# Kernel tuning notes

Hardware: AMD Instinct MI355X
Metric: run time of the kernel (lower is better)

The kernel has to match this reference:

```python
import jax, jax.numpy as jnp
import numpy as np

EPS = 1e-5

def _bn(x, g, b):
    # BatchNorm3d in training mode over (batch, spatial) dims; x: [B, C, N]
    mean = jnp.mean(x, axis=(0, 2), keepdims=True)
    var = jnp.var(x, axis=(0, 2), keepdims=True)
    return g[None, :, None] * (x - mean) * jax.lax.rsqrt(var + EPS) + b[None, :, None]


def setup_inputs() -> dict:
    key = jax.random.key(0)
    ks = jax.random.split(key, 6)
    B, C, N, K, H = 2, 128, 32768, 9, 512
    x = jax.random.normal(ks[0], (B, C, N, 1), dtype=jnp.float32)
    edge_index = jax.random.randint(ks[1], (2, B, N, K), 0, N, dtype=jnp.int32)
    s = 0.05
    return {
        "x": x,
        "edge_index": edge_index,
        "w_mr": jax.random.normal(ks[2], (C, 2 * C), dtype=jnp.float32) * s,
        "b_mr": jnp.zeros((C,), jnp.float32),
        "g_mr": jnp.ones((C,), jnp.float32),
        "be_mr": jnp.zeros((C,), jnp.float32),
        "w1": jax.random.normal(ks[3], (H, C), dtype=jnp.float32) * s,
        "b1": jnp.zeros((H,), jnp.float32),
        "g1": jnp.ones((H,), jnp.float32),
        "be1": jnp.zeros((H,), jnp.float32),
        "w2": jax.random.normal(ks[4], (C, H), dtype=jnp.float32) * s,
        "b2": jnp.zeros((C,), jnp.float32),
        "g2": jnp.ones((C,), jnp.float32),
        "be2": jnp.zeros((C,), jnp.float32),
    }


def reference(x, edge_index, w_mr, b_mr, g_mr, be_mr, w1, b1, g1, be1, w2, b2, g2, be2):
    # x: [B, C, N, 1], edge_index: [2, B, N, K]
    B, C, N, _ = x.shape
    x2 = x[..., 0]  # [B, C, N]

    # batched_index_select: gather node features along N for each (B, N, K) index
    gather = jax.vmap(lambda xb, ib: xb[:, ib])  # ([C,N],[N,K]) -> [C,N,K]
    x_i = gather(x2, edge_index[1])  # [B, C, N, K] center features
    x_j = gather(x2, edge_index[0])  # [B, C, N, K] neighbor features
    rel = jnp.max(x_j - x_i, axis=-1)  # max-relative reduction -> [B, C, N]

    # torch.cat([x.unsqueeze(2), rel.unsqueeze(2)], 2).reshape(B, 2C, N): interleaved channels
    feat = jnp.stack([x2, rel], axis=2).reshape(B, 2 * C, N)

    # BasicConv([2C, C]): Conv3d 1x1 -> BN -> ReLU
    y = jnp.einsum('oc,bcn->bon', w_mr, feat) + b_mr[None, :, None]
    y = jax.nn.relu(_bn(y, g_mr, be_mr))

    # FFN: conv1x1 C->H, BN, ReLU, conv1x1 H->C, BN, residual
    h = jnp.einsum('hc,bcn->bhn', w1, y) + b1[None, :, None]
    h = jax.nn.relu(_bn(h, g1, be1))
    out = jnp.einsum('ch,bhn->bcn', w2, h) + b2[None, :, None]
    out = _bn(out, g2, be2) + y
    return out  # [B, C, N]
```

## Files before the change

### kernel.cpp

```cpp
#include <hip/hip_runtime.h>
#include <hip/hip_bf16.h>
#include <cstddef>
#include <cstdint>

#define BB 2
#define CC 128
#define NN 32768
#define KNBR 9
#define HH 512
#define PP (BB * NN)
#define TWO_C 256
#define EPSBN 1e-5f

typedef __attribute__((ext_vector_type(4))) float f32x4;
typedef __attribute__((ext_vector_type(8))) short s16x8;

__device__ __forceinline__ float bf2f(unsigned int u) {
    return __uint_as_float(u << 16);
}
__device__ __forceinline__ unsigned short f2bf(float f) {
    unsigned int u = __float_as_uint(f);
    u += 0x7fffu + ((u >> 16) & 1u);
    return (unsigned short)(u >> 16);
}

__device__ __forceinline__ s16x8 bnrelu(s16x8 v, f32x4 sa0, f32x4 sa1,
                                        f32x4 sb0, f32x4 sb1) {
    union { s16x8 s; __hip_bfloat162 h[4]; } u;
    u.s = v;
#pragma unroll
    for (int q = 0; q < 4; q++) {
        const float2 f = __bfloat1622float2(u.h[q]);
        const float slo = (q < 2) ? sa0[2 * q] : sa1[2 * q - 4];
        const float shi = (q < 2) ? sa0[2 * q + 1] : sa1[2 * q - 3];
        const float tlo = (q < 2) ? sb0[2 * q] : sb1[2 * q - 4];
        const float thi = (q < 2) ? sb0[2 * q + 1] : sb1[2 * q - 3];
        u.h[q] = __float22bfloat162_rn(make_float2(
            fmaxf(fmaf(slo, f.x, tlo), 0.f), fmaxf(fmaf(shi, f.y, thi), 0.f)));
    }
    return u.s;
}


__global__ __launch_bounds__(256) void transpose_kernel(
    const float* __restrict__ x, unsigned short* __restrict__ xT) {
    __shared__ float t[32][129];
    const int b = blockIdx.y;
    const int n0 = blockIdx.x * 32;
    const int tid = threadIdx.x;
    {
        const int tn = tid % 32;
        const int cq = tid / 32;
        for (int c = cq; c < CC; c += 8)
            t[tn][c] = x[((size_t)b * CC + c) * NN + n0 + tn];
    }
    __syncthreads();
    {
        const int ct = tid % 128;
        const int nq = tid / 128;
        for (int nl = nq; nl < 32; nl += 2)
            xT[((size_t)b * NN + n0 + nl) * CC + ct] = f2bf(t[nl][ct]);
    }
}

__global__ __launch_bounds__(256) void gather_kernel(
    const unsigned short* __restrict__ xT, const int* __restrict__ ei,
    unsigned short* __restrict__ feat) {
    __shared__ unsigned short lds[16 * 264];
    const int p0 = blockIdx.x * 16;
    const int b = p0 >> 15;
    const int n0 = p0 & (NN - 1);
    const int tid = threadIdx.x;
    const int wv = tid >> 6, lane = tid & 63;
    const unsigned short* xb = xT + (size_t)b * NN * CC;

#pragma unroll
    for (int q = 0; q < 4; q++) {
        const int pl = wv * 4 + q;
        const int n = n0 + pl;
        const int* e0 = ei + ((size_t)b * NN + n) * KNBR;
        const int* e1 = ei + ((size_t)(BB + b) * NN + n) * KNBR;
        const unsigned int xv = *(const unsigned int*)(xb + (size_t)n * CC + lane * 2);
        float m0 = -INFINITY, m1 = -INFINITY;
#pragma unroll
        for (int k = 0; k < KNBR; k++) {
            const int j0 = e0[k], j1 = e1[k];
            const unsigned int va = *(const unsigned int*)(xb + (size_t)j0 * CC + lane * 2);
            const unsigned int vb = *(const unsigned int*)(xb + (size_t)j1 * CC + lane * 2);
            m0 = fmaxf(m0, bf2f(va & 0xffffu) - bf2f(vb & 0xffffu));
            m1 = fmaxf(m1, bf2f(va >> 16) - bf2f(vb >> 16));
        }
        ushort4 o;
        o.x = (unsigned short)(xv & 0xffffu);
        o.y = f2bf(m0);
        o.z = (unsigned short)(xv >> 16);
        o.w = f2bf(m1);
        *(ushort4*)(lds + pl * 264 + lane * 4) = o;
    }
    __syncthreads();
#pragma unroll
    for (int pass = 0; pass < 2; pass++) {
        const int s = pass * 256 + tid;
        const int kt = s >> 6, ln = s & 63;
        const int pl = ln & 15, kq = ln >> 4;
        const s16x8 v = *(const s16x8*)(lds + pl * 264 + kt * 32 + kq * 8);
        *(s16x8*)(feat + ((size_t)((p0 >> 4) * 8 + kt) * 64 + ln) * 8) = v;
    }
}

__global__ __launch_bounds__(256) void wconv_kernel(
    const float* __restrict__ w_mr, const float* __restrict__ w1,
    const float* __restrict__ w2, unsigned short* __restrict__ o_mr,
    unsigned short* __restrict__ o1, unsigned short* __restrict__ o2) {
    const int t = blockIdx.x * 256 + threadIdx.x;
    const float* src; unsigned short* dst; int K; int slot;
    if (t < 8192) { src = w1; dst = o1; K = 128; slot = t; }
    else if (t < 16384) { src = w2; dst = o2; K = 512; slot = t - 8192; }
    else if (t < 20480) { src = w_mr; dst = o_mr; K = 256; slot = t - 16384; }
    else return;
    const int lane = slot & 63;
    const int kt = (slot >> 6) % (K / 32);
    const int ot = (slot >> 6) / (K / 32);
    const int oc = ot * 16 + (lane & 15);
    const int k0 = kt * 32 + (lane >> 4) * 8;
    s16x8 v;
#pragma unroll
    for (int j = 0; j < 8; j++) v[j] = (short)f2bf(src[(size_t)oc * K + k0 + j]);
    *(s16x8*)(dst + (size_t)slot * 8) = v;
}

template <int KTOT, int OCB, int OC, bool ACT>
__global__ __launch_bounds__(256) void sgemm_kernel(
    const unsigned short* __restrict__ A,
    const unsigned short* __restrict__ W,
    const float* __restrict__ bias,
    const float* __restrict__ act,
    unsigned short* __restrict__ Cout,
    float* __restrict__ part) {
    constexpr int KT = KTOT / 32;
    constexpr int NTB = OCB / 16;
    constexpr int NTW = NTB / 2;
    constexpr int NL = NTB / 4;
    constexpr int OCT32 = OC / 32;

    __shared__ __align__(16) unsigned short ALDS[4 * KT * 512];
    __shared__ __align__(16) unsigned short WB[2][NTB * 512];

    const int tid = threadIdx.x;
    const int w = tid >> 6, lane = tid & 63;
    const int mw = w >> 1, nw = w & 1;
    const int lm = lane & 15, lg = lane >> 4;
    const int pt0 = blockIdx.x * 4;
    const int ob = blockIdx.y * OCB;

    {
        const unsigned short* Asrc = A + (size_t)pt0 * KT * 512;
        s16x8 ar[KT];
#pragma unroll
        for (int i = 0; i < KT; i++)
            ar[i] = *(const s16x8*)(Asrc + (size_t)(i * 256 + tid) * 8);
        s16x8 wr0[NL];
#pragma unroll
        for (int i = 0; i < NL; i++) {
            const int s = i * 256 + tid, nt = s >> 6, ln = s & 63;
            wr0[i] = *(const s16x8*)(W + ((size_t)(((ob >> 4) + nt) * KT) * 64 + ln) * 8);
        }
#pragma unroll
        for (int i = 0; i < KT; i++)
            *(s16x8*)(ALDS + (size_t)(i * 256 + tid) * 8) = ar[i];
#pragma unroll
        for (int i = 0; i < NL; i++)
            *(s16x8*)(WB[0] + (size_t)(i * 256 + tid) * 8) = wr0[i];
    }
    __syncthreads();

    f32x4 acc[2][NTW] = {};

    for (int kt = 0; kt < KT; kt++) {
        s16x8 wr[NL];
        if (kt + 1 < KT) {
#pragma unroll
            for (int i = 0; i < NL; i++) {
                const int s = i * 256 + tid, nt = s >> 6, ln = s & 63;
                wr[i] = *(const s16x8*)(
                    W + ((size_t)(((ob >> 4) + nt) * KT + kt + 1) * 64 + ln) * 8);
            }
        }
        s16x8 a0 = *(const s16x8*)(ALDS + (size_t)(((mw * 2 + 0) * KT + kt) * 64 + lane) * 8);
        s16x8 a1 = *(const s16x8*)(ALDS + (size_t)(((mw * 2 + 1) * KT + kt) * 64 + lane) * 8);
        if (ACT) {
            const int ke = kt * 32 + lg * 8;
            const f32x4 xa0 = *(const f32x4*)(act + ke);
            const f32x4 xa1 = *(const f32x4*)(act + ke + 4);
            const f32x4 xb0 = *(const f32x4*)(act + KTOT + ke);
            const f32x4 xb1 = *(const f32x4*)(act + KTOT + ke + 4);
            a0 = bnrelu(a0, xa0, xa1, xb0, xb1);
            a1 = bnrelu(a1, xa0, xa1, xb0, xb1);
        }
        const unsigned short* wb = WB[kt & 1];
#pragma unroll
        for (int n = 0; n < NTW; n++) {
            const s16x8 bF = *(const s16x8*)(wb + (size_t)((nw * NTW + n) * 64 + lane) * 8);
            acc[0][n] = __builtin_amdgcn_mfma_f32_16x16x32_bf16(a0, bF, acc[0][n], 0, 0, 0);
            acc[1][n] = __builtin_amdgcn_mfma_f32_16x16x32_bf16(a1, bF, acc[1][n], 0, 0, 0);
        }
        if (kt + 1 < KT) {
#pragma unroll
            for (int i = 0; i < NL; i++)
                *(s16x8*)(WB[(kt + 1) & 1] + (size_t)(i * 256 + tid) * 8) = wr[i];
        }
        __syncthreads();
    }

    float* bs = (float*)ALDS;
    unsigned short* myct = WB[0] + (size_t)w * (NTW / 2) * 512;
    float sA[NTW], sB[NTW], bo[NTW];
#pragma unroll
    for (int n = 0; n < NTW; n++) {
        sA[n] = 0.f; sB[n] = 0.f;
        bo[n] = bias[ob + nw * (OCB / 2) + n * 16 + lm];
    }
#pragma unroll
    for (int mi = 0; mi < 2; mi++) {
        const int ptile = pt0 + mw * 2 + mi;
#pragma unroll
        for (int n = 0; n < NTW; n++) {
            const int lbase = ((n & 1) * 2 + (lm >> 3)) * 16 + lg * 4;
            const int elem = lm & 7;
#pragma unroll
            for (int j = 0; j < 4; j++) {
                const float h = acc[mi][n][j] + bo[n];
                sA[n] += h;
                sB[n] = fmaf(h, h, sB[n]);
                myct[(size_t)((n >> 1) * 64 + lbase + j) * 8 + elem] = f2bf(h);
            }
        }
#pragma unroll
        for (int og = 0; og < NTW / 2; og++) {
            const s16x8 v = *(const s16x8*)(myct + (size_t)(og * 64 + lane) * 8);
            const int oct = ((ob + nw * (OCB / 2)) >> 5) + og;
            *(s16x8*)(Cout + ((size_t)(ptile * OCT32 + oct) * 64 + lane) * 8) = v;
        }
    }
#pragma unroll
    for (int n = 0; n < NTW; n++) {
        float a = sA[n], q = sB[n];
        a += __shfl_xor(a, 16); a += __shfl_xor(a, 32);
        q += __shfl_xor(q, 16); q += __shfl_xor(q, 32);
        if (lg == 0) {
            const int chl = nw * (OCB / 2) + n * 16 + lm;
            bs[(mw * 2 + 0) * OCB + chl] = a;
            bs[(mw * 2 + 1) * OCB + chl] = q;
        }
    }
    __syncthreads();
    if (tid < OCB) {
        const float s = bs[0 * OCB + tid] + bs[2 * OCB + tid];
        const float q = bs[1 * OCB + tid] + bs[3 * OCB + tid];
        const size_t o = ((size_t)blockIdx.y * gridDim.x + blockIdx.x) * 2 * OCB;
        part[o + tid] = s;
        part[o + OCB + tid] = q;
    }
}

template <int OCB, int GX>
__global__ __launch_bounds__(256) void reduce_kernel(
    const float* __restrict__ part, const float* __restrict__ g,
    const float* __restrict__ be, float* __restrict__ act, int OC, float invP) {
    __shared__ float ls[4], lq[4];
    const int c = blockIdx.x;
    const int by = c / OCB, co = c % OCB;
    const int tid = threadIdx.x;
    float s = 0.f, q = 0.f;
#pragma unroll
    for (int i = 0; i < GX / 256; i++) {
        const int bx = i * 256 + tid;
        const size_t o = (size_t)(by * GX + bx) * 2 * OCB;
        s += part[o + co];
        q += part[o + OCB + co];
    }
#pragma unroll
    for (int off = 32; off >= 1; off >>= 1) {
        s += __shfl_xor(s, off);
        q += __shfl_xor(q, off);
    }
    if ((tid & 63) == 0) { ls[tid >> 6] = s; lq[tid >> 6] = q; }
    __syncthreads();
    if (tid == 0) {
        s = ls[0] + ls[1] + ls[2] + ls[3];
        q = lq[0] + lq[1] + lq[2] + lq[3];
        const float mean = s * invP;
        const float var = q * invP - mean * mean;
        const float a = g[c] * rsqrtf(var + EPSBN);
        act[c] = a;
        act[OC + c] = be[c] - mean * a;
    }
}

__global__ __launch_bounds__(256) void final_kernel(
    const unsigned short* __restrict__ yF, const unsigned short* __restrict__ oF,
    const float* __restrict__ act1, const float* __restrict__ act3,
    float* __restrict__ out) {
    __shared__ float t[32][132];
    const int p0 = blockIdx.x * 32;
    const int b = p0 >> 15;
    const int n0 = p0 & (NN - 1);
    const int tid = threadIdx.x;
#pragma unroll
    for (int s = tid; s < 512; s += 256) {
        const int pt = s >> 8;
        const int kt = (s >> 6) & 3;
        const int lane = s & 63;
        const int nl = pt * 16 + (lane & 15);
        const int c0 = kt * 32 + (lane >> 4) * 8;
        const size_t off = ((size_t)(((p0 >> 4) + pt) * 4 + kt) * 64 + lane) * 8;
        const s16x8 yv = *(const s16x8*)(yF + off);
        const s16x8 ov = *(const s16x8*)(oF + off);
        const f32x4 a1lo = *(const f32x4*)(act1 + c0);
        const f32x4 a1hi = *(const f32x4*)(act1 + c0 + 4);
        const f32x4 b1lo = *(const f32x4*)(act1 + CC + c0);
        const f32x4 b1hi = *(const f32x4*)(act1 + CC + c0 + 4);
        const f32x4 a3lo = *(const f32x4*)(act3 + c0);
        const f32x4 a3hi = *(const f32x4*)(act3 + c0 + 4);
        const f32x4 b3lo = *(const f32x4*)(act3 + CC + c0);
        const f32x4 b3hi = *(const f32x4*)(act3 + CC + c0 + 4);
#pragma unroll
        for (int j = 0; j < 8; j++) {
            const float yf = bf2f((unsigned short)yv[j]);
            const float of = bf2f((unsigned short)ov[j]);
            const float a1 = (j < 4) ? a1lo[j] : a1hi[j - 4];
            const float b1 = (j < 4) ? b1lo[j] : b1hi[j - 4];
            const float a3 = (j < 4) ? a3lo[j] : a3hi[j - 4];
            const float b3 = (j < 4) ? b3lo[j] : b3hi[j - 4];
            t[nl][c0 + j] = fmaf(a3, of, b3) + fmaxf(fmaf(a1, yf, b1), 0.f);
        }
    }
    __syncthreads();
    const int tn = tid & 31;
    const int cq = tid >> 5;
    for (int c = cq; c < CC; c += 8)
        out[((size_t)b * CC + c) * NN + n0 + tn] = t[tn][c];
}

extern "C" void kernel_launch(void* const* d_in, const int* in_sizes, int n_in,
                              void* d_out, int out_size, void* d_ws, size_t ws_size,
                              hipStream_t stream) {
    const float* x     = (const float*)d_in[0];
    const int*   ei    = (const int*)d_in[1];
    const float* w_mr  = (const float*)d_in[2];
    const float* b_mr  = (const float*)d_in[3];
    const float* g_mr  = (const float*)d_in[4];
    const float* be_mr = (const float*)d_in[5];
    const float* w1    = (const float*)d_in[6];
    const float* b1    = (const float*)d_in[7];
    const float* g1    = (const float*)d_in[8];
    const float* be1   = (const float*)d_in[9];
    const float* w2    = (const float*)d_in[10];
    const float* b2    = (const float*)d_in[11];
    const float* g2    = (const float*)d_in[12];
    const float* be2   = (const float*)d_in[13];
    float* out = (float*)d_out;

    char* ws = (char*)d_ws;
    unsigned short* xT    = (unsigned short*)(ws + 0);
    unsigned short* featF = (unsigned short*)(ws + 16777216);
    unsigned short* yF    = (unsigned short*)(ws + 50331648);
    unsigned short* hF    = (unsigned short*)(ws + 67108864);
    unsigned short* oF    = (unsigned short*)(ws + 134217728);
    unsigned short* wmrF  = (unsigned short*)(ws + 150994944);
    unsigned short* w1F   = (unsigned short*)(ws + 151060480);
    unsigned short* w2F   = (unsigned short*)(ws + 151191552);
    float* act1  = (float*)(ws + 151322624);
    float* act2  = (float*)(ws + 151323648);
    float* act3  = (float*)(ws + 151327744);
    float* part1 = (float*)(ws + 67108864);
    float* part2 = (float*)(ws + 134217728);
    float* part3 = (float*)(ws + 16777216);

    const float invP = 1.0f / (float)PP;

    transpose_kernel<<<dim3(NN / 32, BB), 256, 0, stream>>>(x, xT);
    gather_kernel<<<PP / 16, 256, 0, stream>>>(xT, ei, featF);
    wconv_kernel<<<80, 256, 0, stream>>>(w_mr, w1, w2, wmrF, w1F, w2F);

    sgemm_kernel<TWO_C, CC, CC, false><<<dim3(PP / 64, 1), 256, 0, stream>>>(
        featF, wmrF, b_mr, act1, yF, part1);
    reduce_kernel<CC, PP / 64><<<CC, 256, 0, stream>>>(
        part1, g_mr, be_mr, act1, CC, invP);

    sgemm_kernel<CC, 256, HH, true><<<dim3(PP / 64, 2), 256, 0, stream>>>(
        yF, w1F, b1, act1, hF, part2);
    reduce_kernel<256, PP / 64><<<HH, 256, 0, stream>>>(
        part2, g1, be1, act2, HH, invP);

    sgemm_kernel<HH, CC, CC, true><<<dim3(PP / 64, 1), 256, 0, stream>>>(
        hF, w2F, b2, act2, oF, part3);
    reduce_kernel<CC, PP / 64><<<CC, 256, 0, stream>>>(
        part3, g2, be2, act3, CC, invP);

    final_kernel<<<PP / 32, 256, 0, stream>>>(yF, oF, act1, act3, out);
}
```

Baseline: 162.3 us.

## Load GEMM weight fragments directly from global memory instead of LDS double buffer

The GEMM kernels no longer stage weight tiles through a double-buffered LDS array with per-k-step barriers. Each wave now reads its weight fragments straight from global memory (expected to hit cache) inside a fully unrolled k loop. A launch-bounds occupancy hint of two blocks is added, and the epilogue buffers are carved from the activation LDS plus a small dedicated float array. This drops the per-iteration syncs and shrinks LDS use, at the cost of more redundant global/L2 weight traffic and more register pressure from the unrolled loads.

```diff
diff --git a/kernel.cpp b/kernel.cpp
--- a/kernel.cpp
+++ b/kernel.cpp
@@ -130,7 +130,7 @@
 }
 
 template <int KTOT, int OCB, int OC, bool ACT>
-__global__ __launch_bounds__(256) void sgemm_kernel(
+__global__ __launch_bounds__(256, 2) void sgemm2_kernel(
     const unsigned short* __restrict__ A,
     const unsigned short* __restrict__ W,
     const float* __restrict__ bias,
@@ -140,11 +140,10 @@
     constexpr int KT = KTOT / 32;
     constexpr int NTB = OCB / 16;
     constexpr int NTW = NTB / 2;
-    constexpr int NL = NTB / 4;
     constexpr int OCT32 = OC / 32;
 
     __shared__ __align__(16) unsigned short ALDS[4 * KT * 512];
-    __shared__ __align__(16) unsigned short WB[2][NTB * 512];
+    __shared__ float bs[4 * OCB];
 
     const int tid = threadIdx.x;
     const int w = tid >> 6, lane = tid & 63;
@@ -159,33 +158,21 @@
 #pragma unroll
         for (int i = 0; i < KT; i++)
             ar[i] = *(const s16x8*)(Asrc + (size_t)(i * 256 + tid) * 8);
-        s16x8 wr0[NL];
-#pragma unroll
-        for (int i = 0; i < NL; i++) {
-            const int s = i * 256 + tid, nt = s >> 6, ln = s & 63;
-            wr0[i] = *(const s16x8*)(W + ((size_t)(((ob >> 4) + nt) * KT) * 64 + ln) * 8);
-        }
 #pragma unroll
         for (int i = 0; i < KT; i++)
             *(s16x8*)(ALDS + (size_t)(i * 256 + tid) * 8) = ar[i];
-#pragma unroll
-        for (int i = 0; i < NL; i++)
-            *(s16x8*)(WB[0] + (size_t)(i * 256 + tid) * 8) = wr0[i];
     }
     __syncthreads();
 
     f32x4 acc[2][NTW] = {};
 
+#pragma unroll
     for (int kt = 0; kt < KT; kt++) {
-        s16x8 wr[NL];
-        if (kt + 1 < KT) {
-#pragma unroll
-            for (int i = 0; i < NL; i++) {
-                const int s = i * 256 + tid, nt = s >> 6, ln = s & 63;
-                wr[i] = *(const s16x8*)(
-                    W + ((size_t)(((ob >> 4) + nt) * KT + kt + 1) * 64 + ln) * 8);
-            }
-        }
+        s16x8 bF[NTW];
+#pragma unroll
+        for (int n = 0; n < NTW; n++)
+            bF[n] = *(const s16x8*)(
+                W + ((size_t)(((ob >> 4) + nw * NTW + n) * KT + kt) * 64 + lane) * 8);
         s16x8 a0 = *(const s16x8*)(ALDS + (size_t)(((mw * 2 + 0) * KT + kt) * 64 + lane) * 8);
         s16x8 a1 = *(const s16x8*)(ALDS + (size_t)(((mw * 2 + 1) * KT + kt) * 64 + lane) * 8);
         if (ACT) {
@@ -197,23 +184,15 @@
             a0 = bnrelu(a0, xa0, xa1, xb0, xb1);
             a1 = bnrelu(a1, xa0, xa1, xb0, xb1);
         }
-        const unsigned short* wb = WB[kt & 1];
 #pragma unroll
         for (int n = 0; n < NTW; n++) {
-            const s16x8 bF = *(const s16x8*)(wb + (size_t)((nw * NTW + n) * 64 + lane) * 8);
-            acc[0][n] = __builtin_amdgcn_mfma_f32_16x16x32_bf16(a0, bF, acc[0][n], 0, 0, 0);
-            acc[1][n] = __builtin_amdgcn_mfma_f32_16x16x32_bf16(a1, bF, acc[1][n], 0, 0, 0);
-        }
-        if (kt + 1 < KT) {
-#pragma unroll
-            for (int i = 0; i < NL; i++)
-                *(s16x8*)(WB[(kt + 1) & 1] + (size_t)(i * 256 + tid) * 8) = wr[i];
-        }
-        __syncthreads();
-    }
-
-    float* bs = (float*)ALDS;
-    unsigned short* myct = WB[0] + (size_t)w * (NTW / 2) * 512;
+            acc[0][n] = __builtin_amdgcn_mfma_f32_16x16x32_bf16(a0, bF[n], acc[0][n], 0, 0, 0);
+            acc[1][n] = __builtin_amdgcn_mfma_f32_16x16x32_bf16(a1, bF[n], acc[1][n], 0, 0, 0);
+        }
+    }
+    __syncthreads();
+
+    unsigned short* myct = ALDS + (size_t)w * (NTW / 2) * 512;
     float sA[NTW], sB[NTW], bo[NTW];
 #pragma unroll
     for (int n = 0; n < NTW; n++) {
@@ -383,17 +362,17 @@
     gather_kernel<<<PP / 16, 256, 0, stream>>>(xT, ei, featF);
     wconv_kernel<<<80, 256, 0, stream>>>(w_mr, w1, w2, wmrF, w1F, w2F);
 
-    sgemm_kernel<TWO_C, CC, CC, false><<<dim3(PP / 64, 1), 256, 0, stream>>>(
+    sgemm2_kernel<TWO_C, CC, CC, false><<<dim3(PP / 64, 1), 256, 0, stream>>>(
         featF, wmrF, b_mr, act1, yF, part1);
     reduce_kernel<CC, PP / 64><<<CC, 256, 0, stream>>>(
         part1, g_mr, be_mr, act1, CC, invP);
 
-    sgemm_kernel<CC, 256, HH, true><<<dim3(PP / 64, 2), 256, 0, stream>>>(
+    sgemm2_kernel<CC, 256, HH, true><<<dim3(PP / 64, 2), 256, 0, stream>>>(
         yF, w1F, b1, act1, hF, part2);
     reduce_kernel<256, PP / 64><<<HH, 256, 0, stream>>>(
         part2, g1, be1, act2, HH, invP);
 
-    sgemm_kernel<HH, CC, CC, true><<<dim3(PP / 64, 1), 256, 0, stream>>>(
+    sgemm2_kernel<HH, CC, CC, true><<<dim3(PP / 64, 1), 256, 0, stream>>>(
         hF, w2F, b2, act2, oF, part3);
     reduce_kernel<CC, PP / 64><<<CC, 256, 0, stream>>>(
         part3, g2, be2, act3, CC, invP);
```

Result: faster. 155.2 us (-4.4%).
